# Performance work log

Hardware: AMD Instinct MI355X
Metric: run time of the kernel (lower is better)

## Reference

```python
import jax, jax.numpy as jnp
import numpy as np

B, T, D, H = 8, 4096, 1024, 8
BW = D // H
MIN_DECAY = 0.001
EPS = 1e-05        # RGLRU eps (clamps)
SCAN_EPS = 1e-07   # closed_form_rnn_scan eps


def setup_inputs() -> dict:
    key = jax.random.key(0)
    k0, k1, k2 = jax.random.split(key, 3)
    x = jax.random.normal(k0, (B, T, D), dtype=jnp.float32)
    a_param = jnp.full((D,), -3.0, dtype=jnp.float32)
    # block-diagonal gate params (orthogonal-ish init approximated by scaled normal)
    w_in = jax.random.normal(k1, (H, BW, BW), dtype=jnp.float32) * (1.0 / np.sqrt(BW))
    b_in = jnp.ones((H, BW), dtype=jnp.float32)
    w_a = jax.random.normal(k2, (H, BW, BW), dtype=jnp.float32) * (1.0 / np.sqrt(BW))
    b_a = jnp.ones((H, BW), dtype=jnp.float32)
    return {"x": x, "a_param": a_param, "w_in": w_in, "b_in": b_in, "w_a": w_a, "b_a": b_a}


def block_diag_linear(x, w, b):
    # x: [B,T,D] -> [B,T,H,BW] ; w: [H,BW,BW] ; b: [H,BW]
    xb = x.reshape(x.shape[:-1] + (H, BW))
    y = jnp.einsum('bthi,hij->bthj', xb, w) + b
    return y.reshape(x.shape)


def closed_form_rnn_scan(x, a):
    # x, a: [B,T,D]; h0 = 0
    a_cumprod = jnp.cumprod(a, axis=1)
    ones = jnp.ones((x.shape[0], 1, x.shape[2]), dtype=x.dtype)
    p_prefix = jnp.concatenate([ones, a_cumprod[:, :-1, :]], axis=1)
    p_prefix = jnp.maximum(p_prefix, SCAN_EPS)
    w = (x + SCAN_EPS) / p_prefix
    S = jnp.cumsum(w, axis=1)
    h = p_prefix * S  # + p_prefix * h0 with h0 = 0
    return h, h[:, -1, :]


def reference(x, a_param, w_in, b_in, w_a, b_a):
    gate_x = jax.nn.sigmoid(block_diag_linear(x, w_in, b_in))
    gate_a = jax.nn.sigmoid(block_diag_linear(x, w_a, b_a))
    log_a = -gate_a * (jax.nn.softplus(a_param) + MIN_DECAY)
    a = jnp.minimum(jnp.exp(log_a), 1.0 - EPS)
    gated_x = x * gate_x
    multiplier = jnp.sqrt(jnp.maximum(1.0 - a * a, EPS))
    normed_x = gated_x * multiplier
    h, _ = closed_form_rnn_scan(normed_x, a)
    return h
```

## Files before the change

### kernel.cpp

```cpp
#include <hip/hip_runtime.h>

#define B_ 8
#define T_ 4096
#define D_ 1024
#define H_ 8
#define BW_ 128
#define NC_ 32
#define CT_ 128
#define EPS7 1e-7f
#define EPS5 1e-5f
#define LOG1MEPS -1.0000186e-05f
#define OMSCALE 256.0f
#define INVOMS 0.00390625f

typedef _Float16 f16x8 __attribute__((ext_vector_type(8)));
typedef _Float16 f16x4 __attribute__((ext_vector_type(4)));
typedef _Float16 f16x2 __attribute__((ext_vector_type(2)));
typedef float f32x4 __attribute__((ext_vector_type(4)));

__global__ __launch_bounds__(256) void k1_gates(
    const float* __restrict__ x, const float* __restrict__ a_param,
    const float* __restrict__ w_in, const float* __restrict__ b_in,
    const float* __restrict__ w_a, const float* __restrict__ b_a,
    f16x2* __restrict__ AU, float* __restrict__ CS)
{
  const int bid  = blockIdx.x;
  const int kc   = bid & (NC_ - 1);
  const int h    = (bid >> 5) & (H_ - 1);
  const int b    = bid >> 8;
  const int tid  = threadIdx.x;
  const int wave = tid >> 6;
  const int lane = tid & 63;
  const int quad = lane >> 4;
  const int l15  = lane & 15;

  __shared__ _Float16 xs[128 * 136];

  const float* xg = x + (size_t)(b * T_ + kc * CT_) * D_ + h * BW_;
  const int jcp = wave * 32 + 2 * l15;

  f16x8 bf[2][2][4];
  #pragma unroll
  for (int g = 0; g < 2; ++g) {
    const float* wptr = (g ? w_a : w_in) + h * BW_ * BW_;
    #pragma unroll
    for (int jt = 0; jt < 2; ++jt) {
      #pragma unroll
      for (int k = 0; k < 4; ++k) {
        const float* wp = wptr + (k * 32 + quad * 8) * BW_ + jcp + jt;
        f16x8 f;
        #pragma unroll
        for (int i = 0; i < 8; ++i) f[i] = (_Float16)wp[i * BW_];
        bf[g][jt][k] = f;
      }
    }
  }
  float bI[2], bA[2], cdec[2];
  #pragma unroll
  for (int jt = 0; jt < 2; ++jt) {
    const int j = h * BW_ + jcp + jt;
    bI[jt] = b_in[j];
    bA[jt] = b_a[j];
    const float ap = a_param[j];
    cdec[jt] = ((ap > 20.f) ? ap : log1pf(__expf(ap))) + 0.001f;
  }

  {
    const int rr = tid >> 5;
    const int cc = (tid & 31) * 4;
    #pragma unroll
    for (int i = 0; i < 16; ++i) {
      const int row = i * 8 + rr;
      const float4 v = *(const float4*)(xg + row * D_ + cc);
      f16x4 hv = { (_Float16)v.x, (_Float16)v.y, (_Float16)v.z, (_Float16)v.w };
      *(f16x4*)(xs + row * 136 + cc) = hv;
    }
  }
  __syncthreads();

  f32x4 acc[2][2][8];
  #pragma unroll
  for (int g = 0; g < 2; ++g)
    #pragma unroll
    for (int jt = 0; jt < 2; ++jt)
      #pragma unroll
      for (int m = 0; m < 8; ++m)
        acc[g][jt][m] = (f32x4){0.f, 0.f, 0.f, 0.f};

  #pragma unroll
  for (int m = 0; m < 8; ++m) {
    f16x8 af[4];
    #pragma unroll
    for (int k = 0; k < 4; ++k)
      af[k] = *(const f16x8*)(xs + (m * 16 + l15) * 136 + k * 32 + quad * 8);
    #pragma unroll
    for (int k = 0; k < 4; ++k)
      #pragma unroll
      for (int g = 0; g < 2; ++g)
        #pragma unroll
        for (int jt = 0; jt < 2; ++jt)
          acc[g][jt][m] = __builtin_amdgcn_mfma_f32_16x16x32_f16(
              af[k], bf[g][jt][k], acc[g][jt][m], 0, 0, 0);
  }

  float sla[2] = {0.f, 0.f};
  const size_t obase = (size_t)(b * T_ + kc * CT_) * D_ + h * BW_ + jcp;
  #pragma unroll
  for (int m = 0; m < 8; ++m) {
    #pragma unroll
    for (int r = 0; r < 4; ++r) {
      const int row = m * 16 + quad * 4 + r;
      const f16x2 xv = *(const f16x2*)(xs + row * 136 + jcp);
      float aenc[2], nxv[2];
      #pragma unroll
      for (int jt = 0; jt < 2; ++jt) {
        const float yi = acc[0][jt][m][r] + bI[jt];
        const float ya = acc[1][jt][m][r] + bA[jt];
        const float gx = __builtin_amdgcn_rcpf(1.f + __expf(-yi));
        const float ga = __builtin_amdgcn_rcpf(1.f + __expf(-ya));
        const float la = -ga * cdec[jt];
        const float a  = fminf(__expf(la), 1.0f - EPS5);
        const float mult = sqrtf(fmaxf(fmaf(-a, a, 1.0f), EPS5));
        aenc[jt] = (1.0f - a) * OMSCALE;
        nxv[jt]  = (float)xv[jt] * gx * mult;
        sla[jt] += fminf(la, LOG1MEPS);
      }
      f16x4 st = { (_Float16)aenc[0], (_Float16)nxv[0],
                   (_Float16)aenc[1], (_Float16)nxv[1] };
      *(f16x4*)&AU[obase + (size_t)row * D_] = st;
    }
  }
  #pragma unroll
  for (int jt = 0; jt < 2; ++jt) {
    sla[jt] += __shfl_xor(sla[jt], 16, 64);
    sla[jt] += __shfl_xor(sla[jt], 32, 64);
  }
  if (quad == 0) {
    const int csb = (b * NC_ + kc) * D_ + h * BW_ + jcp;
    *(float2*)&CS[csb] = make_float2(sla[0], sla[1]);
  }
}

__global__ __launch_bounds__(256) void k2_scan_logs(float* __restrict__ CS)
{
  const int idx = blockIdx.x * 256 + threadIdx.x;
  const int b = idx >> 10;
  const int d = idx & (D_ - 1);
  float lq = 0.f;
  #pragma unroll
  for (int kk = 0; kk < NC_; ++kk) {
    const int o = (b * NC_ + kk) * D_ + d;
    const float c = CS[o];
    CS[o] = lq;
    lq += c;
  }
}

__device__ __forceinline__ float scan_r(float c, float pp, float aprev) {
  return (c > EPS7) ? aprev
                    : ((pp > EPS7) ? (EPS7 * __builtin_amdgcn_rcpf(pp)) : 1.0f);
}

#define SCAN_STEP(f)                                                \
  {                                                                 \
    const float a0 = fmaf((float)(f)[0], -INVOMS, 1.0f);            \
    const float u0 = (float)(f)[1] + EPS7;                          \
    const float a1 = fmaf((float)(f)[2], -INVOMS, 1.0f);            \
    const float u1 = (float)(f)[3] + EPS7;                          \
    const float p0 = fmaxf(c0, EPS7);                               \
    const float r0 = scan_r(c0, pp0, ap0);                          \
    hv0 = fmaf(r0, hv0, u0);                                        \
    const float p1 = fmaxf(c1, EPS7);                               \
    const float r1 = scan_r(c1, pp1, ap1);                          \
    hv1 = fmaf(r1, hv1, u1);                                        \
    rp0 *= r0; rp1 *= r1;                                           \
    c0 *= a0; pp0 = p0; ap0 = a0;                                   \
    c1 *= a1; pp1 = p1; ap1 = a1;                                   \
  }

__global__ __launch_bounds__(256) void k3_summary(
    const f16x2* __restrict__ AU, const float* __restrict__ LQ,
    float* __restrict__ Ak, float* __restrict__ Bk)
{
  const int half = blockIdx.x & 1;
  const int k = (blockIdx.x >> 1) & (NC_ - 1);
  const int b = blockIdx.x >> 6;
  const int d0 = half * 512 + threadIdx.x * 2;
  const size_t base = (size_t)(b * T_ + k * CT_) * D_ + d0;

  float c0, pp0, ap0, c1, pp1, ap1;
  if (k == 0) { c0 = c1 = 1.f; pp0 = pp1 = 1.f; ap0 = ap1 = 1.f; }
  else {
    const float2 lq = *(const float2*)&LQ[(b * NC_ + k) * D_ + d0];
    c0 = __expf(lq.x); c1 = __expf(lq.y);
    const f16x4 ab = *(const f16x4*)&AU[base - D_];
    ap0 = fmaf((float)ab[0], -INVOMS, 1.0f);
    ap1 = fmaf((float)ab[2], -INVOMS, 1.0f);
    pp0 = fmaxf(c0 / ap0, EPS7);
    pp1 = fmaxf(c1 / ap1, EPS7);
  }
  float hv0 = 0.f, hv1 = 0.f, rp0 = 1.f, rp1 = 1.f;

  f16x4 bufA[8], bufB[8];
  #pragma unroll
  for (int i = 0; i < 8; ++i)
    bufA[i] = *(const f16x4*)&AU[base + (size_t)i * D_];

  #pragma unroll 1
  for (int tb = 0; tb < 16; tb += 2) {
    {
      const size_t o = base + (size_t)((tb + 1) * 8) * D_;
      #pragma unroll
      for (int i = 0; i < 8; ++i)
        bufB[i] = *(const f16x4*)&AU[o + (size_t)i * D_];
    }
    #pragma unroll
    for (int i = 0; i < 8; ++i) SCAN_STEP(bufA[i]);
    if (tb < 14) {
      const size_t o = base + (size_t)((tb + 2) * 8) * D_;
      #pragma unroll
      for (int i = 0; i < 8; ++i)
        bufA[i] = *(const f16x4*)&AU[o + (size_t)i * D_];
    }
    #pragma unroll
    for (int i = 0; i < 8; ++i) SCAN_STEP(bufB[i]);
  }
  const int o = (b * NC_ + k) * D_ + d0;
  *(float2*)&Ak[o] = make_float2(rp0, rp1);
  *(float2*)&Bk[o] = make_float2(hv0, hv1);
}

__global__ __launch_bounds__(256) void k3_carry(
    float* __restrict__ Ak, const float* __restrict__ Bk)
{
  const int idx = blockIdx.x * 256 + threadIdx.x;
  const int b = idx >> 10;
  const int d = idx & (D_ - 1);
  float Hv = 0.f;
  #pragma unroll
  for (int kk = 0; kk < NC_; ++kk) {
    const int o = (b * NC_ + kk) * D_ + d;
    const float Av = Ak[o];
    Ak[o] = Hv;
    Hv = fmaf(Av, Hv, Bk[o]);
  }
}

#define SCAN_STEP_ST(f, t)                                          \
  {                                                                 \
    const float a0 = fmaf((float)(f)[0], -INVOMS, 1.0f);            \
    const float u0 = (float)(f)[1] + EPS7;                          \
    const float a1 = fmaf((float)(f)[2], -INVOMS, 1.0f);            \
    const float u1 = (float)(f)[3] + EPS7;                          \
    const float p0 = fmaxf(c0, EPS7);                               \
    const float r0 = scan_r(c0, pp0, ap0);                          \
    hv0 = fmaf(r0, hv0, u0);                                        \
    const float p1 = fmaxf(c1, EPS7);                               \
    const float r1 = scan_r(c1, pp1, ap1);                          \
    hv1 = fmaf(r1, hv1, u1);                                        \
    *(float2*)&op[(size_t)(t) * D_] = make_float2(hv0, hv1);        \
    c0 *= a0; pp0 = p0; ap0 = a0;                                   \
    c1 *= a1; pp1 = p1; ap1 = a1;                                   \
  }

__global__ __launch_bounds__(256) void k3_scan(
    const f16x2* __restrict__ AU, const float* __restrict__ LQ,
    const float* __restrict__ Hc, float* __restrict__ out)
{
  const int half = blockIdx.x & 1;
  const int k = (blockIdx.x >> 1) & (NC_ - 1);
  const int b = blockIdx.x >> 6;
  const int d0 = half * 512 + threadIdx.x * 2;
  const size_t base = (size_t)(b * T_ + k * CT_) * D_ + d0;
  float* __restrict__ op = out + base;

  float c0, pp0, ap0, c1, pp1, ap1;
  if (k == 0) { c0 = c1 = 1.f; pp0 = pp1 = 1.f; ap0 = ap1 = 1.f; }
  else {
    const float2 lq = *(const float2*)&LQ[(b * NC_ + k) * D_ + d0];
    c0 = __expf(lq.x); c1 = __expf(lq.y);
    const f16x4 ab = *(const f16x4*)&AU[base - D_];
    ap0 = fmaf((float)ab[0], -INVOMS, 1.0f);
    ap1 = fmaf((float)ab[2], -INVOMS, 1.0f);
    pp0 = fmaxf(c0 / ap0, EPS7);
    pp1 = fmaxf(c1 / ap1, EPS7);
  }
  float hv0, hv1;
  {
    const float2 hc = *(const float2*)&Hc[(b * NC_ + k) * D_ + d0];
    hv0 = hc.x; hv1 = hc.y;
  }

  f16x4 bufA[8], bufB[8];
  #pragma unroll
  for (int i = 0; i < 8; ++i)
    bufA[i] = *(const f16x4*)&AU[base + (size_t)i * D_];

  #pragma unroll 1
  for (int tb = 0; tb < 16; tb += 2) {
    {
      const size_t o = base + (size_t)((tb + 1) * 8) * D_;
      #pragma unroll
      for (int i = 0; i < 8; ++i)
        bufB[i] = *(const f16x4*)&AU[o + (size_t)i * D_];
    }
    #pragma unroll
    for (int i = 0; i < 8; ++i) SCAN_STEP_ST(bufA[i], tb * 8 + i);
    if (tb < 14) {
      const size_t o = base + (size_t)((tb + 2) * 8) * D_;
      #pragma unroll
      for (int i = 0; i < 8; ++i)
        bufA[i] = *(const f16x4*)&AU[o + (size_t)i * D_];
    }
    #pragma unroll
    for (int i = 0; i < 8; ++i) SCAN_STEP_ST(bufB[i], (tb + 1) * 8 + i);
  }
}

extern "C" void kernel_launch(void* const* d_in, const int* in_sizes, int n_in,
                              void* d_out, int out_size, void* d_ws, size_t ws_size,
                              hipStream_t stream) {
  const float* x       = (const float*)d_in[0];
  const float* a_param = (const float*)d_in[1];
  const float* w_in    = (const float*)d_in[2];
  const float* b_in    = (const float*)d_in[3];
  const float* w_a     = (const float*)d_in[4];
  const float* b_a     = (const float*)d_in[5];
  float* out = (float*)d_out;

  char* ws = (char*)d_ws;
  f16x2* AU = (f16x2*)ws;
  float* CS = (float*)(ws + (size_t)B_ * T_ * D_ * 4);
  float* Ak = CS + B_ * NC_ * D_;
  float* Bk = Ak + B_ * NC_ * D_;

  k1_gates<<<B_ * H_ * NC_, 256, 0, stream>>>(x, a_param, w_in, b_in, w_a, b_a,
                                              AU, CS);
  k2_scan_logs<<<(B_ * D_) / 256, 256, 0, stream>>>(CS);
  k3_summary<<<B_ * NC_ * 2, 256, 0, stream>>>(AU, CS, Ak, Bk);
  k3_carry<<<(B_ * D_) / 256, 256, 0, stream>>>(Ak, Bk);
  k3_scan<<<B_ * NC_ * 2, 256, 0, stream>>>(AU, CS, Ak, out);
}
```

Baseline: 367.6 us.

## Load gate GEMM operands directly from global and split scan blocks finer

The gate kernel no longer stages the x tile through shared memory with a barrier. Each lane now reads its MFMA A-fragments and its epilogue x values straight from global memory as float4/float2 and converts them to half in registers. This removes LDS traffic and the sync, but it issues redundant, less coalesced global loads that rely on cache hits. Separately, the summary and scan kernels now run with 128-thread blocks and twice as many blocks, giving the GPU more blocks to spread across its compute units.

Result: slower. 427.4 us (+16.3%).

```diff
diff --git a/kernel.cpp b/kernel.cpp
--- a/kernel.cpp
+++ b/kernel.cpp
@@ -34,8 +34,6 @@
   const int quad = lane >> 4;
   const int l15  = lane & 15;
 
-  __shared__ _Float16 xs[128 * 136];
-
   const float* xg = x + (size_t)(b * T_ + kc * CT_) * D_ + h * BW_;
   const int jcp = wave * 32 + 2 * l15;
 
@@ -65,19 +63,6 @@
     cdec[jt] = ((ap > 20.f) ? ap : log1pf(__expf(ap))) + 0.001f;
   }
 
-  {
-    const int rr = tid >> 5;
-    const int cc = (tid & 31) * 4;
-    #pragma unroll
-    for (int i = 0; i < 16; ++i) {
-      const int row = i * 8 + rr;
-      const float4 v = *(const float4*)(xg + row * D_ + cc);
-      f16x4 hv = { (_Float16)v.x, (_Float16)v.y, (_Float16)v.z, (_Float16)v.w };
-      *(f16x4*)(xs + row * 136 + cc) = hv;
-    }
-  }
-  __syncthreads();
-
   f32x4 acc[2][2][8];
   #pragma unroll
   for (int g = 0; g < 2; ++g)
@@ -91,8 +76,16 @@
   for (int m = 0; m < 8; ++m) {
     f16x8 af[4];
     #pragma unroll
-    for (int k = 0; k < 4; ++k)
-      af[k] = *(const f16x8*)(xs + (m * 16 + l15) * 136 + k * 32 + quad * 8);
+    for (int k = 0; k < 4; ++k) {
+      const float* xp = xg + (size_t)(m * 16 + l15) * D_ + k * 32 + quad * 8;
+      const float4 v0 = *(const float4*)xp;
+      const float4 v1 = *(const float4*)(xp + 4);
+      f16x8 f = { (_Float16)v0.x, (_Float16)v0.y,
+                  (_Float16)v0.z, (_Float16)v0.w,
+                  (_Float16)v1.x, (_Float16)v1.y,
+                  (_Float16)v1.z, (_Float16)v1.w };
+      af[k] = f;
+    }
     #pragma unroll
     for (int k = 0; k < 4; ++k)
       #pragma unroll
@@ -110,7 +103,8 @@
     #pragma unroll
     for (int r = 0; r < 4; ++r) {
       const int row = m * 16 + quad * 4 + r;
-      const f16x2 xv = *(const f16x2*)(xs + row * 136 + jcp);
+      const float2 xv = *(const float2*)(xg + (size_t)row * D_ + jcp);
+      const float xq[2] = {xv.x, xv.y};
       float aenc[2], nxv[2];
       #pragma unroll
       for (int jt = 0; jt < 2; ++jt) {
@@ -122,7 +116,7 @@
         const float a  = fminf(__expf(la), 1.0f - EPS5);
         const float mult = sqrtf(fmaxf(fmaf(-a, a, 1.0f), EPS5));
         aenc[jt] = (1.0f - a) * OMSCALE;
-        nxv[jt]  = (float)xv[jt] * gx * mult;
+        nxv[jt]  = xq[jt] * gx * mult;
         sla[jt] += fminf(la, LOG1MEPS);
       }
       f16x4 st = { (_Float16)aenc[0], (_Float16)nxv[0],
@@ -178,14 +172,14 @@
     c1 *= a1; pp1 = p1; ap1 = a1;                                   \
   }
 
-__global__ __launch_bounds__(256) void k3_summary(
+__global__ __launch_bounds__(128) void k3_summary(
     const f16x2* __restrict__ AU, const float* __restrict__ LQ,
     float* __restrict__ Ak, float* __restrict__ Bk)
 {
-  const int half = blockIdx.x & 1;
-  const int k = (blockIdx.x >> 1) & (NC_ - 1);
-  const int b = blockIdx.x >> 6;
-  const int d0 = half * 512 + threadIdx.x * 2;
+  const int q = blockIdx.x & 3;
+  const int k = (blockIdx.x >> 2) & (NC_ - 1);
+  const int b = blockIdx.x >> 7;
+  const int d0 = q * 256 + threadIdx.x * 2;
   const size_t base = (size_t)(b * T_ + k * CT_) * D_ + d0;
 
   float c0, pp0, ap0, c1, pp1, ap1;
@@ -263,14 +257,14 @@
     c1 *= a1; pp1 = p1; ap1 = a1;                                   \
   }
 
-__global__ __launch_bounds__(256) void k3_scan(
+__global__ __launch_bounds__(128) void k3_scan(
     const f16x2* __restrict__ AU, const float* __restrict__ LQ,
     const float* __restrict__ Hc, float* __restrict__ out)
 {
-  const int half = blockIdx.x & 1;
-  const int k = (blockIdx.x >> 1) & (NC_ - 1);
-  const int b = blockIdx.x >> 6;
-  const int d0 = half * 512 + threadIdx.x * 2;
+  const int q = blockIdx.x & 3;
+  const int k = (blockIdx.x >> 2) & (NC_ - 1);
+  const int b = blockIdx.x >> 7;
+  const int d0 = q * 256 + threadIdx.x * 2;
   const size_t base = (size_t)(b * T_ + k * CT_) * D_ + d0;
   float* __restrict__ op = out + base;
 
@@ -337,7 +331,7 @@
   k1_gates<<<B_ * H_ * NC_, 256, 0, stream>>>(x, a_param, w_in, b_in, w_a, b_a,
                                               AU, CS);
   k2_scan_logs<<<(B_ * D_) / 256, 256, 0, stream>>>(CS);
-  k3_summary<<<B_ * NC_ * 2, 256, 0, stream>>>(AU, CS, Ak, Bk);
+  k3_summary<<<B_ * NC_ * 4, 128, 0, stream>>>(AU, CS, Ak, Bk);
   k3_carry<<<(B_ * D_) / 256, 256, 0, stream>>>(Ak, Bk);
-  k3_scan<<<B_ * NC_ * 2, 256, 0, stream>>>(AU, CS, Ak, out);
-}
+  k3_scan<<<B_ * NC_ * 4, 128, 0, stream>>>(AU, CS, Ak, out);
+}
```
